# Performance work log

Hardware: AMD Instinct MI355X
Metric: run time of the kernel (lower is better)

Reference implementation:

```python
import jax, jax.numpy as jnp
import numpy as np

B, H, W, C = 4, 48, 48, 256
NUM_HEADS = 8
DEPTH = C // NUM_HEADS  # 32


def setup_inputs() -> dict:
    key = jax.random.key(0)
    ks = jax.random.split(key, 8)
    scale = 1.0 / np.sqrt(C)
    return {
        "inputs": jax.random.normal(ks[0], (B, H, W, C), dtype=jnp.float32),
        "wq": jax.random.normal(ks[1], (C, C), dtype=jnp.float32) * scale,
        "bq": jax.random.normal(ks[2], (C,), dtype=jnp.float32) * 0.01,
        "wk": jax.random.normal(ks[3], (C, C), dtype=jnp.float32) * scale,
        "bk": jax.random.normal(ks[4], (C,), dtype=jnp.float32) * 0.01,
        "wv": jax.random.normal(ks[5], (C, C), dtype=jnp.float32) * scale,
        "bv": jax.random.normal(ks[6], (C,), dtype=jnp.float32) * 0.01,
        "gamma": jax.random.normal(ks[7], (), dtype=jnp.float32) * 0.1,
    }


def reference(inputs, wq, bq, wk, bk, wv, bv, gamma):
    b, h, w, c = inputs.shape
    n = h * w  # number of tokens

    def proj_split(wm, bm):
        # 1x1 conv == per-pixel dense: [b,h,w,c] @ [c,c] + bias
        y = jnp.einsum('bhwc,cd->bhwd', inputs, wm) + bm
        # split heads -> [b, num_heads, n, depth]
        return y.reshape(b, n, NUM_HEADS, DEPTH).transpose(0, 2, 1, 3)

    q = proj_split(wq, bq) / jnp.sqrt(jnp.asarray(DEPTH, inputs.dtype))
    k = proj_split(wk, bk)
    v = proj_split(wv, bv)

    s = jnp.einsum('bnqd,bnkd->bnqk', q, k)        # [b, heads, n, n]
    a = jax.nn.softmax(s, axis=-1)
    o = jnp.einsum('bnqk,bnkd->bnqd', a, v)        # [b, heads, n, depth]
    o = o.transpose(0, 2, 1, 3).reshape(b, h, w, c)
    return gamma * o + inputs
```

## Files before the change

### kernel.cpp

```cpp
#include <hip/hip_runtime.h>
#include <hip/hip_bf16.h>
#include <cstdint>

#define B_    4
#define NH    8
#define N_TOK 2304
#define D_    32
#define C_    256
#define M_ROWS (B_ * N_TOK)
#define KVB   128
#define NT2   (N_TOK / KVB)
#define M_FIX 10.0f

typedef float  f32x4  __attribute__((ext_vector_type(4)));
typedef short  bf16x8 __attribute__((ext_vector_type(8)));

#define GLOADLDS(g, l) __builtin_amdgcn_global_load_lds( \
    (const __attribute__((address_space(1))) unsigned*)(g), \
    (__attribute__((address_space(3))) unsigned*)(l), 16, 0, 0)

static __device__ __forceinline__ unsigned short f2bf(float f) {
    union { float f; unsigned u; } v; v.f = f;
    unsigned u = v.u;
    u += 0x7FFF + ((u >> 16) & 1);
    return (unsigned short)(u >> 16);
}

static __device__ __forceinline__ unsigned cvt_pk_bf16(float a, float b) {
    unsigned r;
    asm("v_cvt_pk_bf16_f32 %0, %1, %2" : "=v"(r) : "v"(a), "v"(b));
    return r;
}

__global__ void k_prep_x(const float* __restrict__ x, unsigned short* __restrict__ xb) {
    int i = blockIdx.x * blockDim.x + threadIdx.x;
    float4 v = reinterpret_cast<const float4*>(x)[i];
    ushort4 o;
    o.x = f2bf(v.x); o.y = f2bf(v.y); o.z = f2bf(v.z); o.w = f2bf(v.w);
    reinterpret_cast<ushort4*>(xb)[i] = o;
}

__global__ void k_prep_w(const float* __restrict__ w0, const float* __restrict__ w1,
                         const float* __restrict__ w2, unsigned short* __restrict__ wt) {
    __shared__ float tile[64][65];
    int mat = blockIdx.y;
    const float* w = (mat == 0) ? w0 : (mat == 1) ? w1 : w2;
    int t   = blockIdx.x;
    int tc  = (t & 3) * 64;
    int td  = (t >> 2) * 64;
    int tid = threadIdx.x;
    int r0  = tid >> 6;
    int x0  = tid & 63;
#pragma unroll
    for (int it = 0; it < 16; ++it) {
        int c = it * 4 + r0;
        tile[c][x0] = w[(tc + c) * C_ + td + x0];
    }
    __syncthreads();
    unsigned short* wto = wt + mat * (C_ * C_);
#pragma unroll
    for (int it = 0; it < 16; ++it) {
        int d = it * 4 + r0;
        wto[(td + d) * C_ + tc + x0] = f2bf(tile[x0][d]);
    }
}

__global__ __launch_bounds__(256) void k_proj(
    const unsigned short* __restrict__ xb,
    const unsigned short* __restrict__ wtb,
    const float* __restrict__ bq, const float* __restrict__ bk, const float* __restrict__ bv,
    unsigned short* __restrict__ qo, unsigned short* __restrict__ ko, unsigned short* __restrict__ vto)
{
    __shared__ __align__(16) unsigned short A_lds[2][64][32];
    __shared__ __align__(16) unsigned short B_lds[2][128][32];

    int rows0 = blockIdx.x * 64;
    int cols0 = blockIdx.y * 128;
    int mat   = cols0 >> 8;
    const float* bias = (mat == 0) ? bq : (mat == 1) ? bk : bv;
    float scale = (mat == 0) ? (0.17677669529663687f * 1.4426950408889634f) : 1.0f;

    int tid = threadIdx.x, wave = tid >> 6, lane = tid & 63;
    int lr = lane & 15, lg = lane >> 4;
    int wr = wave >> 1, wc = wave & 1;

    int srow = lane >> 2, sslot = lane & 3;
    int ra   = wave * 16 + srow;
    int keyA = ((ra >> 1) & 1) | (((ra >> 3) & 1) << 1);
    const unsigned short* asrc = xb + (rows0 + ra) * C_ + ((sslot ^ keyA) * 8);
    int rb   = wave * 32 + srow;
    int keyB0 = ((rb >> 1) & 1) | (((rb >> 3) & 1) << 1);
    int keyB1 = (((rb + 16) >> 1) & 1) | ((((rb + 16) >> 3) & 1) << 1);
    const unsigned short* bsrc0 = wtb + (cols0 + rb) * C_ + ((sslot ^ keyB0) * 8);
    const unsigned short* bsrc1 = wtb + (cols0 + rb + 16) * C_ + ((sslot ^ keyB1) * 8);

    char* aldsb = (char*)&A_lds[0][0][0];
    char* bldsb = (char*)&B_lds[0][0][0];
    int adst = wave * 1024;
    int bdst0 = wave * 2048, bdst1 = bdst0 + 1024;

    int xorb = (((lr >> 1) & 1) << 4) | (((lr >> 3) & 1) << 5);
    int fcol = (lg * 16) ^ xorb;
    int arow0 = wr * 32 + lr;
    int brow0 = wc * 64 + lr;

    GLOADLDS(asrc, aldsb + adst);
    GLOADLDS(bsrc0, bldsb + bdst0);
    GLOADLDS(bsrc1, bldsb + bdst1);
    __syncthreads();

    f32x4 acc[2][4];
#pragma unroll
    for (int i = 0; i < 2; ++i)
#pragma unroll
        for (int j = 0; j < 4; ++j) acc[i][j] = (f32x4){0.f, 0.f, 0.f, 0.f};

    int buf = 0;
    for (int ks = 0; ks < 8; ++ks) {
        if (ks < 7) {
            int ko_ = (ks + 1) * 32;
            char* ad = aldsb + (buf ^ 1) * 4096;
            char* bd = bldsb + (buf ^ 1) * 8192;
            GLOADLDS(asrc + ko_, ad + adst);
            GLOADLDS(bsrc0 + ko_, bd + bdst0);
            GLOADLDS(bsrc1 + ko_, bd + bdst1);
        }
        const char* ac = aldsb + buf * 4096;
        const char* bc = bldsb + buf * 8192;

        bf16x8 a[2], b[4];
#pragma unroll
        for (int fr = 0; fr < 2; ++fr)
            a[fr] = *reinterpret_cast<const bf16x8*>(ac + (arow0 + fr * 16) * 64 + fcol);
#pragma unroll
        for (int fn = 0; fn < 4; ++fn)
            b[fn] = *reinterpret_cast<const bf16x8*>(bc + (brow0 + fn * 16) * 64 + fcol);

        __builtin_amdgcn_s_setprio(1);
#pragma unroll
        for (int fr = 0; fr < 2; ++fr)
#pragma unroll
            for (int fn = 0; fn < 4; ++fn)
                acc[fr][fn] = __builtin_amdgcn_mfma_f32_16x16x32_bf16(a[fr], b[fn], acc[fr][fn], 0, 0, 0);
        __builtin_amdgcn_s_setprio(0);

        __syncthreads();
        buf ^= 1;
    }

    int bidx = rows0 / N_TOK;
    int nb   = rows0 - bidx * N_TOK + wr * 32 + lg * 4;

    if (mat == 2) {
#pragma unroll
        for (int fr = 0; fr < 2; ++fr)
#pragma unroll
            for (int fn = 0; fn < 4; ++fn) {
                int cm = (cols0 & 255) + wc * 64 + fn * 16 + lr;
                float bsv = bias[cm];
                int hh = cm >> 5, d = cm & 31;
                uint2 pr;
                pr.x = cvt_pk_bf16(acc[fr][fn][0] + bsv, acc[fr][fn][1] + bsv);
                pr.y = cvt_pk_bf16(acc[fr][fn][2] + bsv, acc[fr][fn][3] + bsv);
                *reinterpret_cast<uint2*>(vto + ((bidx * NH + hh) * D_ + d) * N_TOK + nb + fr * 16) = pr;
            }
    } else {
        unsigned short* dst = (mat == 0) ? qo : ko;
#pragma unroll
        for (int fr = 0; fr < 2; ++fr)
#pragma unroll
            for (int fn = 0; fn < 4; ++fn) {
                int cm = (cols0 & 255) + wc * 64 + fn * 16 + lr;
                float bsv = bias[cm];
                int hh = cm >> 5, d = cm & 31;
#pragma unroll
                for (int j = 0; j < 4; ++j) {
                    float val = (acc[fr][fn][j] + bsv) * scale;
                    dst[((bidx * NH + hh) * N_TOK + nb + fr * 16 + j) * D_ + d] = f2bf(val);
                }
            }
    }
}

__global__ __launch_bounds__(256) void k_attn(
    const unsigned short* __restrict__ qb,
    const unsigned short* __restrict__ kb,
    const unsigned short* __restrict__ vtg,
    const float* __restrict__ x,
    const float* __restrict__ gamma_p,
    float* __restrict__ out)
{
    __shared__ __align__(16) unsigned short K_lds[2][KVB][32];
    __shared__ __align__(16) unsigned short Vt_lds[2][32][KVB];

    int wid = (blockIdx.x & 7) * 144 + (blockIdx.x >> 3);
    int bh  = wid / 36;
    int qb0 = (wid % 36) * 64;

    int tid = threadIdx.x, wave = tid >> 6, lane = tid & 63;
    int lr = lane & 15, lg = lane >> 4;

    const unsigned short* Q  = qb  + bh * N_TOK * D_;
    const unsigned short* K  = kb  + bh * N_TOK * D_;
    const unsigned short* Vt = vtg + bh * D_ * N_TOK;

    int qrow = qb0 + wave * 16 + lr;
    bf16x8 q_frag = *reinterpret_cast<const bf16x8*>(Q + qrow * D_ + lg * 8);

    int c0   = wave * 2;
    int kr0  = 16 * c0 + (lane >> 2);
    int kslot = ((kr0 >> 1) & 1) | (((kr0 >> 3) & 1) << 1);
    int koff0 = kr0 * D_ + (((lane & 3) ^ kslot) * 8);
    int koff1 = koff0 + 16 * D_;
    int vr0   = 8 * wave + (lane >> 4);
    int voff0 = vr0 * N_TOK + (((lane & 15) ^ (vr0 & 7)) * 8);
    int voff1 = (vr0 + 4) * N_TOK + (((lane & 15) ^ ((vr0 + 4) & 7)) * 8);

    char* kldsb = (char*)&K_lds[0][0][0];
    char* vldsb = (char*)&Vt_lds[0][0][0];
    int dst0 = c0 * 1024, dst1 = dst0 + 1024;

    GLOADLDS(K + koff0, kldsb + dst0);
    GLOADLDS(K + koff1, kldsb + dst1);
    GLOADLDS(Vt + voff0, vldsb + dst0);
    GLOADLDS(Vt + voff1, vldsb + dst1);
    __syncthreads();

    f32x4 acc0  = (f32x4){0.f, 0.f, 0.f, 0.f};
    f32x4 acc1  = (f32x4){0.f, 0.f, 0.f, 0.f};
    f32x4 acc_l = (f32x4){0.f, 0.f, 0.f, 0.f};

    union { unsigned w[4]; bf16x8 v; } ones;
    ones.w[0] = 0x3F803F80u; ones.w[1] = 0x3F803F80u;
    ones.w[2] = 0x3F803F80u; ones.w[3] = 0x3F803F80u;

    int kread_key = (((lr >> 1) & 1) << 4) | (((lr >> 2) & 1) << 5);
    int krow_lane = (8 * (lr >> 2) + (lr & 3)) * 64 + ((lg * 16) ^ kread_key);
    int vkey = (lr & 7) << 4;

    const f32x4 zinit = (f32x4){-M_FIX, -M_FIX, -M_FIX, -M_FIX};

    int buf = 0;
    for (int t = 0; t < NT2; ++t) {
        if (t < NT2 - 1) {
            const unsigned short* Kn = K + (t + 1) * (KVB * D_);
            const unsigned short* Vn = Vt + (t + 1) * KVB;
            char* kd = kldsb + (buf ^ 1) * 8192;
            char* vd = vldsb + (buf ^ 1) * 8192;
            GLOADLDS(Kn + koff0, kd + dst0);
            GLOADLDS(Kn + koff1, kd + dst1);
            GLOADLDS(Vn + voff0, vd + dst0);
            GLOADLDS(Vn + voff1, vd + dst1);
        }
        const char* kc = kldsb + buf * 8192;
        const char* vc = vldsb + buf * 8192;

        f32x4 s[8];
        __builtin_amdgcn_s_setprio(1);
#pragma unroll
        for (int kt = 0; kt < 8; ++kt) {
            bf16x8 kf = *reinterpret_cast<const bf16x8*>(
                kc + (kt >> 1) * 2048 + (kt & 1) * 256 + krow_lane);
            s[kt] = __builtin_amdgcn_mfma_f32_16x16x32_bf16(kf, q_frag, zinit, 0, 0, 0);
        }
        __builtin_amdgcn_s_setprio(0);

#pragma unroll
        for (int kt = 0; kt < 8; ++kt)
#pragma unroll
            for (int j = 0; j < 4; ++j)
                s[kt][j] = __builtin_amdgcn_exp2f(s[kt][j]);

        __builtin_amdgcn_s_setprio(1);
#pragma unroll
        for (int kseg = 0; kseg < 4; ++kseg) {
            union { unsigned w[4]; bf16x8 v; } pa;
            pa.w[0] = cvt_pk_bf16(s[2 * kseg][0],     s[2 * kseg][1]);
            pa.w[1] = cvt_pk_bf16(s[2 * kseg][2],     s[2 * kseg][3]);
            pa.w[2] = cvt_pk_bf16(s[2 * kseg + 1][0], s[2 * kseg + 1][1]);
            pa.w[3] = cvt_pk_bf16(s[2 * kseg + 1][2], s[2 * kseg + 1][3]);
            int off = (kseg * 64 + lg * 16) ^ vkey;
            bf16x8 vf0 = *reinterpret_cast<const bf16x8*>(vc + lr * 256 + off);
            bf16x8 vf1 = *reinterpret_cast<const bf16x8*>(vc + (16 + lr) * 256 + off);
            acc0  = __builtin_amdgcn_mfma_f32_16x16x32_bf16(pa.v, vf0,    acc0,  0, 0, 0);
            acc1  = __builtin_amdgcn_mfma_f32_16x16x32_bf16(pa.v, vf1,    acc1,  0, 0, 0);
            acc_l = __builtin_amdgcn_mfma_f32_16x16x32_bf16(pa.v, ones.v, acc_l, 0, 0, 0);
        }
        __builtin_amdgcn_s_setprio(0);

        __syncthreads();
        buf ^= 1;
    }

    float g = gamma_p[0];
    int b = bh >> 3, head = bh & 7;
#pragma unroll
    for (int j = 0; j < 4; ++j) {
        float linv = 1.0f / acc_l[j];
        int n = qb0 + wave * 16 + 4 * lg + j;
        long r = (long)(b * N_TOK + n) * C_ + head * 32;
        out[r + lr]      = g * (acc0[j] * linv) + x[r + lr];
        out[r + 16 + lr] = g * (acc1[j] * linv) + x[r + 16 + lr];
    }
}

extern "C" void kernel_launch(void* const* d_in, const int* in_sizes, int n_in,
                              void* d_out, int out_size, void* d_ws, size_t ws_size,
                              hipStream_t stream) {
    const float* x     = (const float*)d_in[0];
    const float* wq    = (const float*)d_in[1];
    const float* bq    = (const float*)d_in[2];
    const float* wk    = (const float*)d_in[3];
    const float* bk    = (const float*)d_in[4];
    const float* wv    = (const float*)d_in[5];
    const float* bv    = (const float*)d_in[6];
    const float* gamma = (const float*)d_in[7];
    float* out = (float*)d_out;

    char* ws = (char*)d_ws;
    unsigned short* xb   = (unsigned short*)(ws);
    unsigned short* wt   = (unsigned short*)(ws + 4718592);
    unsigned short* qbuf = (unsigned short*)(ws + 5111808);
    unsigned short* kbuf = (unsigned short*)(ws + 9830400);
    unsigned short* vtg  = (unsigned short*)(ws + 14548992);

    k_prep_x<<<dim3(M_ROWS * C_ / 1024), dim3(256), 0, stream>>>(x, xb);
    k_prep_w<<<dim3(16, 3), dim3(256), 0, stream>>>(wq, wk, wv, wt);
    k_proj<<<dim3(M_ROWS / 64, 6), dim3(256), 0, stream>>>(xb, wt, bq, bk, bv, qbuf, kbuf, vtg);
    k_attn<<<dim3(N_TOK / 64 * B_ * NH), dim3(256), 0, stream>>>(qbuf, kbuf, vtg, x, gamma, out);
}
```

Before: 68.64 us.

## Use 512-thread attention blocks with split K/V staging waves and interleaved exp

The attention kernel now uses 8 waves per block, each handling 16 query rows, so a block covers 128 queries and every K/V tile staged in shared memory serves twice as many queries. Half the waves load the K tile and half load the V tile, replacing the old scheme where every wave loaded both. The exp2 step is moved inside the P·V loop so exponentials for each segment can overlap with the MFMAs, and the priority raise around the P·V MFMAs is dropped. The aim is to cut global and LDS traffic per query and shorten register live ranges, at the cost of fewer blocks (576) and larger barrier groups.

```diff
diff --git a/kernel.cpp b/kernel.cpp
--- a/kernel.cpp
+++ b/kernel.cpp
@@ -182,7 +182,7 @@
     }
 }
 
-__global__ __launch_bounds__(256) void k_attn(
+__global__ __launch_bounds__(512, 8) void k_attn(
     const unsigned short* __restrict__ qb,
     const unsigned short* __restrict__ kb,
     const unsigned short* __restrict__ vtg,
@@ -193,9 +193,9 @@
     __shared__ __align__(16) unsigned short K_lds[2][KVB][32];
     __shared__ __align__(16) unsigned short Vt_lds[2][32][KVB];
 
-    int wid = (blockIdx.x & 7) * 144 + (blockIdx.x >> 3);
-    int bh  = wid / 36;
-    int qb0 = (wid % 36) * 64;
+    int wid = (blockIdx.x & 7) * 72 + (blockIdx.x >> 3);
+    int bh  = wid / 18;
+    int qb0 = (wid % 18) * 128;
 
     int tid = threadIdx.x, wave = tid >> 6, lane = tid & 63;
     int lr = lane & 15, lg = lane >> 4;
@@ -207,12 +207,14 @@
     int qrow = qb0 + wave * 16 + lr;
     bf16x8 q_frag = *reinterpret_cast<const bf16x8*>(Q + qrow * D_ + lg * 8);
 
-    int c0   = wave * 2;
-    int kr0  = 16 * c0 + (lane >> 2);
+    bool stK = wave < 4;
+    int  sw  = stK ? wave : (wave - 4);
+    int c0   = sw * 2;
+    int kr0  = 32 * sw + (lane >> 2);
     int kslot = ((kr0 >> 1) & 1) | (((kr0 >> 3) & 1) << 1);
     int koff0 = kr0 * D_ + (((lane & 3) ^ kslot) * 8);
     int koff1 = koff0 + 16 * D_;
-    int vr0   = 8 * wave + (lane >> 4);
+    int vr0   = 8 * sw + (lane >> 4);
     int voff0 = vr0 * N_TOK + (((lane & 15) ^ (vr0 & 7)) * 8);
     int voff1 = (vr0 + 4) * N_TOK + (((lane & 15) ^ ((vr0 + 4) & 7)) * 8);
 
@@ -220,10 +222,13 @@
     char* vldsb = (char*)&Vt_lds[0][0][0];
     int dst0 = c0 * 1024, dst1 = dst0 + 1024;
 
-    GLOADLDS(K + koff0, kldsb + dst0);
-    GLOADLDS(K + koff1, kldsb + dst1);
-    GLOADLDS(Vt + voff0, vldsb + dst0);
-    GLOADLDS(Vt + voff1, vldsb + dst1);
+    if (stK) {
+        GLOADLDS(K + koff0, kldsb + dst0);
+        GLOADLDS(K + koff1, kldsb + dst1);
+    } else {
+        GLOADLDS(Vt + voff0, vldsb + dst0);
+        GLOADLDS(Vt + voff1, vldsb + dst1);
+    }
     __syncthreads();
 
     f32x4 acc0  = (f32x4){0.f, 0.f, 0.f, 0.f};
@@ -243,14 +248,17 @@
     int buf = 0;
     for (int t = 0; t < NT2; ++t) {
         if (t < NT2 - 1) {
-            const unsigned short* Kn = K + (t + 1) * (KVB * D_);
-            const unsigned short* Vn = Vt + (t + 1) * KVB;
-            char* kd = kldsb + (buf ^ 1) * 8192;
-            char* vd = vldsb + (buf ^ 1) * 8192;
-            GLOADLDS(Kn + koff0, kd + dst0);
-            GLOADLDS(Kn + koff1, kd + dst1);
-            GLOADLDS(Vn + voff0, vd + dst0);
-            GLOADLDS(Vn + voff1, vd + dst1);
+            if (stK) {
+                const unsigned short* Kn = K + (t + 1) * (KVB * D_);
+                char* kd = kldsb + (buf ^ 1) * 8192;
+                GLOADLDS(Kn + koff0, kd + dst0);
+                GLOADLDS(Kn + koff1, kd + dst1);
+            } else {
+                const unsigned short* Vn = Vt + (t + 1) * KVB;
+                char* vd = vldsb + (buf ^ 1) * 8192;
+                GLOADLDS(Vn + voff0, vd + dst0);
+                GLOADLDS(Vn + voff1, vd + dst1);
+            }
         }
         const char* kc = kldsb + buf * 8192;
         const char* vc = vldsb + buf * 8192;
@@ -266,19 +274,20 @@
         __builtin_amdgcn_s_setprio(0);
 
 #pragma unroll
-        for (int kt = 0; kt < 8; ++kt)
-#pragma unroll
-            for (int j = 0; j < 4; ++j)
-                s[kt][j] = __builtin_amdgcn_exp2f(s[kt][j]);
-
-        __builtin_amdgcn_s_setprio(1);
-#pragma unroll
         for (int kseg = 0; kseg < 4; ++kseg) {
+            float e0 = __builtin_amdgcn_exp2f(s[2 * kseg][0]);
+            float e1 = __builtin_amdgcn_exp2f(s[2 * kseg][1]);
+            float e2 = __builtin_amdgcn_exp2f(s[2 * kseg][2]);
+            float e3 = __builtin_amdgcn_exp2f(s[2 * kseg][3]);
+            float e4 = __builtin_amdgcn_exp2f(s[2 * kseg + 1][0]);
+            float e5 = __builtin_amdgcn_exp2f(s[2 * kseg + 1][1]);
+            float e6 = __builtin_amdgcn_exp2f(s[2 * kseg + 1][2]);
+            float e7 = __builtin_amdgcn_exp2f(s[2 * kseg + 1][3]);
             union { unsigned w[4]; bf16x8 v; } pa;
-            pa.w[0] = cvt_pk_bf16(s[2 * kseg][0],     s[2 * kseg][1]);
-            pa.w[1] = cvt_pk_bf16(s[2 * kseg][2],     s[2 * kseg][3]);
-            pa.w[2] = cvt_pk_bf16(s[2 * kseg + 1][0], s[2 * kseg + 1][1]);
-            pa.w[3] = cvt_pk_bf16(s[2 * kseg + 1][2], s[2 * kseg + 1][3]);
+            pa.w[0] = cvt_pk_bf16(e0, e1);
+            pa.w[1] = cvt_pk_bf16(e2, e3);
+            pa.w[2] = cvt_pk_bf16(e4, e5);
+            pa.w[3] = cvt_pk_bf16(e6, e7);
             int off = (kseg * 64 + lg * 16) ^ vkey;
             bf16x8 vf0 = *reinterpret_cast<const bf16x8*>(vc + lr * 256 + off);
             bf16x8 vf1 = *reinterpret_cast<const bf16x8*>(vc + (16 + lr) * 256 + off);
@@ -286,7 +295,6 @@
             acc1  = __builtin_amdgcn_mfma_f32_16x16x32_bf16(pa.v, vf1,    acc1,  0, 0, 0);
             acc_l = __builtin_amdgcn_mfma_f32_16x16x32_bf16(pa.v, ones.v, acc_l, 0, 0, 0);
         }
-        __builtin_amdgcn_s_setprio(0);
 
         __syncthreads();
         buf ^= 1;
@@ -327,5 +335,5 @@
     k_prep_x<<<dim3(M_ROWS * C_ / 1024), dim3(256), 0, stream>>>(x, xb);
     k_prep_w<<<dim3(16, 3), dim3(256), 0, stream>>>(wq, wk, wv, wt);
     k_proj<<<dim3(M_ROWS / 64, 6), dim3(256), 0, stream>>>(xb, wt, bq, bk, bv, qbuf, kbuf, vtg);
-    k_attn<<<dim3(N_TOK / 64 * B_ * NH), dim3(256), 0, stream>>>(qbuf, kbuf, vtg, x, gamma, out);
-}
+    k_attn<<<dim3(N_TOK / 128 * B_ * NH), dim3(512), 0, stream>>>(qbuf, kbuf, vtg, x, gamma, out);
+}
```

Measured after the change: 69.55 us. Within noise of the previous version (+1.3%).
